# Kernel tuning notes

Measured on AMD Instinct MI355X. Metric: run time of the kernel, lower is better.

The kernel has to match this reference:

```python
import jax, jax.numpy as jnp
import numpy as np

G = 512          # number of graphs
N = 512          # nodes per graph (equal-sized graphs)
NN = G * N       # total nodes
EG = 8192        # edges per graph (avg degree 16)
C_IN, HID, OUT, K = 128, 32, 2, 20
LATENT = HID * 2 + 1  # 65 = conv1 kernel size & stride


def _gcn(x, W, b, src, dst, deg_inv_sqrt):
    """GCNConv with self-loops: out = D^-1/2 (A+I) D^-1/2 (x W) + b."""
    h = x @ W                                        # [NN, out]
    norm = deg_inv_sqrt[src] * deg_inv_sqrt[dst]     # [E]
    agg = jnp.zeros_like(h).at[dst].add(h[src] * norm[:, None])
    # self-loop message: norm_ii = deg_inv_sqrt[i]^2
    agg = agg + h * (deg_inv_sqrt * deg_inv_sqrt)[:, None]
    return agg + b


def setup_inputs() -> dict:
    key = jax.random.key(0)
    ks = jax.random.split(key, 24)
    x = jax.random.normal(ks[0], (NN, C_IN), jnp.float32)
    offs = (jnp.arange(G, dtype=jnp.int32) * N)[:, None]
    src = (jax.random.randint(ks[1], (G, EG), 0, N, jnp.int32) + offs).reshape(-1)
    dst = (jax.random.randint(ks[2], (G, EG), 0, N, jnp.int32) + offs).reshape(-1)
    edge_index = jnp.stack([src, dst])               # [2, G*EG]
    batch = jnp.repeat(jnp.arange(G, dtype=jnp.int32), N)

    def lin(k, fan_in, shape):
        return jax.random.normal(k, shape, jnp.float32) / np.sqrt(fan_in)

    return {
        "x": x, "edge_index": edge_index, "batch": batch,
        "W0": lin(ks[3], C_IN, (C_IN, HID)), "b0": jnp.zeros((HID,), jnp.float32),
        "W1": lin(ks[4], HID, (HID, HID)),   "b1": jnp.zeros((HID,), jnp.float32),
        "W2": lin(ks[5], HID, (HID, 1)),     "b2": jnp.zeros((1,), jnp.float32),
        "conv1_w": lin(ks[6], LATENT, (16, 1, LATENT)), "conv1_b": jnp.zeros((16,), jnp.float32),
        "conv2_w": lin(ks[7], 16 * 5, (32, 16, 5)),     "conv2_b": jnp.zeros((32,), jnp.float32),
        "lin1_w": lin(ks[8], 192, (192, 128)), "lin1_b": jnp.zeros((128,), jnp.float32),
        "lin2_w": lin(ks[9], 128, (128, OUT)), "lin2_b": jnp.zeros((OUT,), jnp.float32),
    }


def reference(x, edge_index, batch, W0, b0, W1, b1, W2, b2,
              conv1_w, conv1_b, conv2_w, conv2_b,
              lin1_w, lin1_b, lin2_w, lin2_b):
    src, dst = edge_index[0], edge_index[1]
    deg = jnp.zeros((NN,), jnp.float32).at[dst].add(1.0) + 1.0  # +1 self-loop
    dis = jax.lax.rsqrt(deg)

    x1 = jnp.tanh(_gcn(x,  W0, b0, src, dst, dis))   # [NN, 32]
    x2 = jnp.tanh(_gcn(x1, W1, b1, src, dst, dis))   # [NN, 32]
    x3 = jnp.tanh(_gcn(x2, W2, b2, src, dst, dis))   # [NN, 1]
    feat = jnp.concatenate([x1, x2, x3], axis=-1)    # [NN, 65]

    # global_sort_pool: equal-sized contiguous graphs -> reshape, sort by last
    # channel (descending) within each graph, take top-k nodes.
    fg = feat.reshape(G, N, LATENT)
    idx = jnp.argsort(-fg[..., -1], axis=1)[:, :K]                 # [G, K]
    pooled = jnp.take_along_axis(fg, idx[:, :, None], axis=1)      # [G, K, 65]

    # conv1: Conv1d(1,16,kernel=65,stride=65) over flattened [G,1,K*65]
    # == per-sorted-node matmul with the 65-wide kernel.
    h = jax.nn.relu(jnp.einsum('gkc,oc->gok', pooled, conv1_w[:, 0, :])
                    + conv1_b[None, :, None])                      # [G, 16, K]
    h = h.reshape(G, 16, K // 2, 2).max(-1)                        # MaxPool1d(2,2) -> [G,16,10]
    h = jax.nn.relu(
        jax.lax.conv_general_dilated(h, conv2_w, (1,), 'VALID',
                                     dimension_numbers=('NCH', 'OIH', 'NCH'))
        + conv2_b[None, :, None])                                  # [G, 32, 6]
    h = h.reshape(G, -1)                                           # [G, 192]
    h = jax.nn.relu(h @ lin1_w + lin1_b)
    # dropout is identity in eval mode
    return h @ lin2_w + lin2_b                                     # [G, 2]
```

## Files before the change

kernel.cpp:

```cpp
#include <hip/hip_runtime.h>
#include <math.h>

#define G_ 512
#define N_ 512
#define NN_ (G_*N_)
#define EG_ 8192
#define EGP 8704
#define CIN_ 128
#define HID_ 32
#define K_ 20
#define LAT_ 65
#define NSTRIPE 4
#define SW 8
#define HP 513

#define EPS_REL 1.8e-7f

__device__ __forceinline__ void decode_swz(int f, int& g, int& st) {
    int xcd = f & 7;
    int q = f >> 3;
    st = q & 3;
    g = xcd + 8 * (q >> 2);
}

__global__ __launch_bounds__(512) void csr2_kernel(const int* __restrict__ src,
                                                   const int* __restrict__ dst,
                                                   unsigned short* __restrict__ srcl,
                                                   int* __restrict__ gstart,
                                                   unsigned short* __restrict__ nperm,
                                                   double* __restrict__ disd) {
    __shared__ int cnt[N_];
    __shared__ int startv[N_];
    __shared__ int tmpv[N_];
    __shared__ int cursor[N_];
    __shared__ int hcur[128];
    __shared__ unsigned short binE[EGP];
    int g = blockIdx.x, tid = threadIdx.x;
    const int* ds = dst + (size_t)g * EG_;
    const int* ss = src + (size_t)g * EG_;
    int nb = g * N_;

    cnt[tid] = 0;
    if (tid < 128) hcur[tid] = 0;
    for (int i = tid; i < EGP; i += 512) binE[i] = 0xFFFF;
    __syncthreads();
    for (int e = tid; e < EG_; e += 512) atomicAdd(&cnt[ds[e] - nb], 1);
    __syncthreads();

    int mydeg = cnt[tid];
    int db = mydeg < 127 ? mydeg : 127;
    atomicAdd(&hcur[db], 1);
    __syncthreads();
    if (tid == 0) {
        int run = 0;
        for (int d = 0; d < 128; ++d) { int v = hcur[d]; hcur[d] = run; run += v; }
    }
    __syncthreads();
    {
        int slot = atomicAdd(&hcur[db], 1);
        nperm[g * N_ + slot] = (unsigned short)tid;
    }

    int pc = (mydeg + 1) & ~1;
    startv[tid] = pc;
    __syncthreads();
    for (int off = 1; off < N_; off <<= 1) {
        tmpv[tid] = startv[tid] + (tid >= off ? startv[tid - off] : 0);
        __syncthreads();
        startv[tid] = tmpv[tid];
        __syncthreads();
    }

    int excl = startv[tid] - pc;
    cursor[tid] = excl;
    gstart[g * (N_ + 1) + tid] = excl;
    if (tid == 511) gstart[g * (N_ + 1) + N_] = startv[511];
    disd[nb + tid] = 1.0 / sqrt((double)(mydeg + 1));
    __syncthreads();

    for (int e = tid; e < EG_; e += 512) {
        int d = ds[e] - nb;
        int slot = atomicAdd(&cursor[d], 1);
        binE[slot] = (unsigned short)e;
    }
    __syncthreads();

    {
        int n = mydeg;
        for (int i = 1; i < n; ++i) {
            unsigned short key = binE[excl + i];
            int j = i - 1;
            while (j >= 0 && binE[excl + j] > key) {
                binE[excl + j + 1] = binE[excl + j];
                --j;
            }
            binE[excl + j + 1] = key;
        }
    }
    __syncthreads();

    for (int i = tid; i < EGP; i += 512) {
        unsigned short e = binE[i];
        srcl[(size_t)g * EGP + i] =
            (e == 0xFFFF) ? (unsigned short)N_ : (unsigned short)(ss[e] - nb);
    }
}

template <int CI>
__global__ __launch_bounds__(256) void mm_kernel(const float* __restrict__ xin,
                                                 const float* __restrict__ W,
                                                 double* __restrict__ h) {
    __shared__ float sx[64][CI + 4];
    __shared__ float sWt[HID_][CI + 5];
    int tid = threadIdx.x;
    for (int i = tid; i < CI * HID_; i += 256) {
        int c = i / HID_, o = i % HID_;
        sWt[o][c] = W[i];
    }
    size_t base = (size_t)blockIdx.x * 64;
    const float4* xsrc = (const float4*)(xin + base * CI);
    for (int i = tid; i < 64 * CI / 4; i += 256) {
        int row = i / (CI / 4), col = (i % (CI / 4)) * 4;
        *(float4*)&sx[row][col] = xsrc[i];
    }
    __syncthreads();

    int o2 = tid & 15, q = tid >> 4;
    int n0 = q * 4;
    double acc[4][2];
#pragma unroll
    for (int j = 0; j < 4; ++j) { acc[j][0] = 0.0; acc[j][1] = 0.0; }

    for (int c = 0; c < CI; c += 4) {
        float4 wa = *(const float4*)&sWt[2 * o2][c];
        float4 wb = *(const float4*)&sWt[2 * o2 + 1][c];
        double w0a = (double)wa.x, w1a = (double)wa.y,
               w2a = (double)wa.z, w3a = (double)wa.w;
        double w0b = (double)wb.x, w1b = (double)wb.y,
               w2b = (double)wb.z, w3b = (double)wb.w;
#pragma unroll
        for (int j = 0; j < 4; ++j) {
            float4 v = *(const float4*)&sx[n0 + j][c];
            double vx = (double)v.x, vy = (double)v.y,
                   vz = (double)v.z, vw = (double)v.w;
            acc[j][0] = fma(vx, w0a, acc[j][0]);
            acc[j][0] = fma(vy, w1a, acc[j][0]);
            acc[j][0] = fma(vz, w2a, acc[j][0]);
            acc[j][0] = fma(vw, w3a, acc[j][0]);
            acc[j][1] = fma(vx, w0b, acc[j][1]);
            acc[j][1] = fma(vy, w1b, acc[j][1]);
            acc[j][1] = fma(vz, w2b, acc[j][1]);
            acc[j][1] = fma(vw, w3b, acc[j][1]);
        }
    }
    int stripe = o2 >> 3;
    {
        int o = 2 * o2;
        int strp = o >> 3;
        int oc = o & 7;
#pragma unroll
        for (int j = 0; j < 4; ++j) {
            double2 val;
            val.x = acc[j][0];
            val.y = acc[j][1];
            *(double2*)&h[(((size_t)strp) * NN_ + base + n0 + j) * SW + oc] = val;
        }
    }
    (void)stripe;
}

__global__ __launch_bounds__(512) void agg_kernel(const double* __restrict__ h,
                                                  const unsigned short* __restrict__ srcl,
                                                  const int* __restrict__ gstart,
                                                  const unsigned short* __restrict__ nperm,
                                                  const double* __restrict__ disd,
                                                  const float* __restrict__ bias,
                                                  float* __restrict__ xoutf) {
    __shared__ double hd2[SW * HP];
    __shared__ unsigned short ssrc[EGP];
    __shared__ unsigned short sstart[N_ + 2];
    __shared__ unsigned short sperm[N_];
    int g, st, tid = threadIdx.x;
    decode_swz(blockIdx.x, g, st);
    size_t nbase = (size_t)g * N_;

    for (int i = tid; i < EGP; i += 512) ssrc[i] = srcl[(size_t)g * EGP + i];
    for (int i = tid; i <= N_; i += 512) sstart[i] = (unsigned short)gstart[g * (N_ + 1) + i];
    sperm[tid] = nperm[g * N_ + tid];
    __syncthreads();

    const double* hraw = h + ((size_t)st * NN_ + nbase) * SW;
    const double* dg = disd + nbase;
    for (int i = tid; i < N_ * SW; i += 512) {
        int s = i >> 3, oc = i & 7;
        hd2[oc * HP + s] = hraw[i] * dg[s];
    }
    if (tid < SW) hd2[tid * HP + N_] = -0.0;
    __syncthreads();

    int oc = tid & 7, grp = tid >> 3;
    const double* hrow = hd2 + oc * HP;
    const unsigned int* ssrc32 = (const unsigned int*)ssrc;
    double b = (double)bias[st * SW + oc];

    int nn[8], e0h[8], e1h[8];
    double a[8];
    int mx = 0;
#pragma unroll
    for (int j = 0; j < 8; ++j) {
        int n = sperm[grp * 8 + j];
        nn[j] = n;
        e0h[j] = sstart[n] >> 1;
        e1h[j] = sstart[n + 1] >> 1;
        a[j] = 0.0;
        int d = e1h[j] - e0h[j];
        mx = d > mx ? d : mx;
    }
    for (int t = 0; t < mx; ++t) {
#pragma unroll
        for (int j = 0; j < 8; ++j) {
            int idx = e0h[j] + t;
            if (idx < e1h[j]) {
                unsigned int pr = ssrc32[idx];
                a[j] += hrow[pr & 0xFFFFu];
                a[j] += hrow[pr >> 16];
            }
        }
    }
#pragma unroll
    for (int j = 0; j < 8; ++j) {
        int n = nn[j];
        double dn = dg[n];
        double v = a[j] * dn + hrow[n] * dn + b;
        xoutf[(nbase + n) * HID_ + st * SW + oc] = tanhf((float)v);
    }
}

__global__ __launch_bounds__(512) void agg_mm_kernel(
        const float* __restrict__ xin,
        const float* __restrict__ W,
        const unsigned short* __restrict__ srcl,
        const int* __restrict__ gstart,
        const unsigned short* __restrict__ nperm,
        const double* __restrict__ disd,
        const float* __restrict__ bias,
        float* __restrict__ xoutf) {
    __shared__ double hd2[SW * HP];
    __shared__ unsigned short ssrc[EGP];
    __shared__ unsigned short sstart[N_ + 2];
    __shared__ double sWd[HID_ * SW];
    int g, st, tid = threadIdx.x;
    decode_swz(blockIdx.x, g, st);
    size_t nbase = (size_t)g * N_;

    for (int i = tid; i < EGP; i += 512) ssrc[i] = srcl[(size_t)g * EGP + i];
    for (int i = tid; i <= N_; i += 512) sstart[i] = (unsigned short)gstart[g * (N_ + 1) + i];
    if (tid < HID_ * SW) {
        int c = tid >> 3, oc = tid & 7;
        sWd[tid] = (double)W[c * HID_ + st * SW + oc];
    }
    __syncthreads();

    const double* dg = disd + nbase;
    {
        int s = tid;
        const float4* xr4 = (const float4*)(xin + (nbase + s) * HID_);
        float xrow[HID_];
#pragma unroll
        for (int q = 0; q < HID_ / 4; ++q) {
            float4 v = xr4[q];
            xrow[q * 4 + 0] = v.x;
            xrow[q * 4 + 1] = v.y;
            xrow[q * 4 + 2] = v.z;
            xrow[q * 4 + 3] = v.w;
        }
        double a[SW];
#pragma unroll
        for (int oc = 0; oc < SW; ++oc) a[oc] = 0.0;
#pragma unroll
        for (int c = 0; c < HID_; ++c) {
            double xv = (double)xrow[c];
#pragma unroll
            for (int oc = 0; oc < SW; ++oc)
                a[oc] = fma(xv, sWd[c * SW + oc], a[oc]);
        }
        double ds = dg[s];
#pragma unroll
        for (int oc = 0; oc < SW; ++oc)
            hd2[oc * HP + s] = a[oc] * ds;
    }
    if (tid < SW) hd2[tid * HP + N_] = -0.0;
    __syncthreads();

    int oc = tid & 7, grp = tid >> 3;
    const double* hrow = hd2 + oc * HP;
    const unsigned int* ssrc32 = (const unsigned int*)ssrc;
    double b = (double)bias[st * SW + oc];

    int nn[8], e0h[8], e1h[8];
    double a[8];
    int mx = 0;
#pragma unroll
    for (int j = 0; j < 8; ++j) {
        int n = nperm[g * N_ + grp * 8 + j];
        nn[j] = n;
        e0h[j] = sstart[n] >> 1;
        e1h[j] = sstart[n + 1] >> 1;
        a[j] = 0.0;
        int d = e1h[j] - e0h[j];
        mx = d > mx ? d : mx;
    }
    for (int t = 0; t < mx; ++t) {
#pragma unroll
        for (int j = 0; j < 8; ++j) {
            int idx = e0h[j] + t;
            if (idx < e1h[j]) {
                unsigned int pr = ssrc32[idx];
                a[j] += hrow[pr & 0xFFFFu];
                a[j] += hrow[pr >> 16];
            }
        }
    }
#pragma unroll
    for (int j = 0; j < 8; ++j) {
        int n = nn[j];
        double dn = dg[n];
        double v = a[j] * dn + hrow[n] * dn + b;
        xoutf[(nbase + n) * HID_ + st * SW + oc] = tanhf((float)v);
    }
}

__global__ __launch_bounds__(512) void gcn3_head_kernel(
        const float* __restrict__ xin,
        const float* __restrict__ W2,
        const float* __restrict__ b2,
        const unsigned short* __restrict__ srcl,
        const int* __restrict__ gstart,
        const double* __restrict__ disd,
        const float* __restrict__ x1,
        const float* __restrict__ x2,
        const float* __restrict__ c1w, const float* __restrict__ c1b,
        const float* __restrict__ c2w, const float* __restrict__ c2b,
        const float* __restrict__ l1w, const float* __restrict__ l1b,
        const float* __restrict__ l2w, const float* __restrict__ l2b,
        float* __restrict__ out) {
    __shared__ double h1[N_ + 1];
    __shared__ unsigned short ssrc[EGP];
    __shared__ int sstart[N_ + 1];
    __shared__ double sdis[N_ + 1];
    __shared__ float sv[N_];
    __shared__ int   topk[K_];
    __shared__ float pooled[K_][LAT_];
    __shared__ float c1[16][K_];
    __shared__ float mp[16][10];
    __shared__ float c2s[32 * 6];
    __shared__ float l1s[128];
    int g = blockIdx.x, tid = threadIdx.x;
    size_t nbase = (size_t)g * N_;

    for (int i = tid; i < EGP; i += 512) ssrc[i] = srcl[(size_t)g * EGP + i];
    for (int i = tid; i <= N_; i += 512) sstart[i] = gstart[g * (N_ + 1) + i];
    if (tid == 0) { h1[N_] = -0.0; sdis[N_] = 1.0; }
    if (tid < K_) topk[tid] = tid;
    int n = tid;
    {
        double a = 0.0;
#pragma unroll
        for (int c = 0; c < HID_; ++c)
            a = fma((double)xin[(nbase + n) * HID_ + c], (double)W2[c], a);
        h1[n] = a;
        sdis[n] = disd[nbase + n];
    }
    __syncthreads();

    {
        int e0 = sstart[n], e1 = sstart[n + 1];
        double a = 0.0;
        for (int e = e0; e < e1; ++e) {
            int s = ssrc[e];
            a += h1[s] * sdis[s];
        }
        double dn = sdis[n];
        double v = a * dn + h1[n] * dn * dn + (double)b2[0];
        sv[n] = (float)tanh(v);
    }
    __syncthreads();

    {
        float v = sv[n];
        int rank = 0;
        for (int j = 0; j < N_; ++j) {
            float u = sv[j];
            float mag = fmaxf(fabsf(u), fabsf(v));
            bool tie = fabsf(u - v) <= EPS_REL * mag;
            bool beats = tie ? (j < n) : (u > v);
            rank += beats;
        }
        if (rank < K_) topk[rank] = n;
    }
    __syncthreads();

    for (int i = tid; i < K_ * LAT_; i += 512) {
        int k = i / LAT_, c = i % LAT_;
        int node = topk[k];
        float f;
        if (c < HID_)            f = x1[(nbase + node) * HID_ + c];
        else if (c < 2 * HID_)   f = x2[(nbase + node) * HID_ + (c - HID_)];
        else                     f = sv[node];
        pooled[k][c] = f;
    }
    __syncthreads();

    for (int i = tid; i < 16 * K_; i += 512) {
        int o = i / K_, k = i % K_;
        float acc = c1b[o];
        for (int c = 0; c < LAT_; ++c) acc += pooled[k][c] * c1w[o * LAT_ + c];
        c1[o][k] = fmaxf(acc, 0.f);
    }
    __syncthreads();

    for (int i = tid; i < 160; i += 512) {
        int o = i / 10, t = i % 10;
        mp[o][t] = fmaxf(c1[o][2 * t], c1[o][2 * t + 1]);
    }
    __syncthreads();

    for (int i = tid; i < 192; i += 512) {
        int o = i / 6, t = i % 6;
        float acc = c2b[o];
        for (int ic = 0; ic < 16; ++ic)
#pragma unroll
            for (int j = 0; j < 5; ++j)
                acc += mp[ic][t + j] * c2w[(o * 16 + ic) * 5 + j];
        c2s[o * 6 + t] = fmaxf(acc, 0.f);
    }
    __syncthreads();

    for (int i = tid; i < 128; i += 512) {
        float acc = l1b[i];
        for (int c = 0; c < 192; ++c) acc += c2s[c] * l1w[c * 128 + i];
        l1s[i] = fmaxf(acc, 0.f);
    }
    __syncthreads();

    for (int i = tid; i < 2; i += 512) {
        float acc = l2b[i];
        for (int c = 0; c < 128; ++c) acc += l1s[c] * l2w[c * 2 + i];
        out[g * 2 + i] = acc;
    }
}

extern "C" void kernel_launch(void* const* d_in, const int* in_sizes, int n_in,
                              void* d_out, int out_size, void* d_ws, size_t ws_size,
                              hipStream_t stream) {
    const float* x   = (const float*)d_in[0];
    const int*   ei  = (const int*)d_in[1];
    const float* W0  = (const float*)d_in[3];
    const float* b0  = (const float*)d_in[4];
    const float* W1  = (const float*)d_in[5];
    const float* b1  = (const float*)d_in[6];
    const float* W2  = (const float*)d_in[7];
    const float* b2  = (const float*)d_in[8];
    const float* c1w = (const float*)d_in[9];
    const float* c1b = (const float*)d_in[10];
    const float* c2w = (const float*)d_in[11];
    const float* c2b = (const float*)d_in[12];
    const float* l1w = (const float*)d_in[13];
    const float* l1b = (const float*)d_in[14];
    const float* l2w = (const float*)d_in[15];
    const float* l2b = (const float*)d_in[16];

    const int* src = ei;
    const int* dst = ei + (size_t)G_ * EG_;

    char* wsb = (char*)d_ws;
    double* h64  = (double*)wsb;                 wsb += (size_t)NN_ * HID_ * 8;
    unsigned short* srcl = (unsigned short*)wsb; wsb += (size_t)G_ * EGP * 2;
    int* gstart = (int*)wsb;                     wsb += (size_t)G_ * (N_ + 1) * 4;
    unsigned short* nperm = (unsigned short*)wsb; wsb += (size_t)G_ * N_ * 2;
    double* disd = (double*)wsb;                 wsb += (size_t)NN_ * 8;
    float*  x1f  = (float*)wsb;                  wsb += (size_t)NN_ * HID_ * 4;
    float*  x2f  = (float*)wsb;                  wsb += (size_t)NN_ * HID_ * 4;

    csr2_kernel<<<G_, 512, 0, stream>>>(src, dst, srcl, gstart, nperm, disd);
    mm_kernel<CIN_><<<NN_ / 64, 256, 0, stream>>>(x, W0, h64);
    agg_kernel<<<G_ * NSTRIPE, 512, 0, stream>>>(h64, srcl, gstart, nperm, disd, b0, x1f);
    agg_mm_kernel<<<G_ * NSTRIPE, 512, 0, stream>>>(x1f, W1, srcl, gstart, nperm, disd, b1, x2f);
    gcn3_head_kernel<<<G_, 512, 0, stream>>>(x2f, W2, b2, srcl, gstart, disd,
                                             x1f, x2f, c1w, c1b, c2w, c2b,
                                             l1w, l1b, l2w, l2b, (float*)d_out);
}
```

Measured before the change: 323.2 us.

## Merge CSR build and first matmul into one launch with block-range dispatch

Fuses the independent CSR-construction kernel and the first-layer fp64 matmul into a single launch. The first G blocks build the CSR and the remaining blocks compute x@W0, so the two phases can run concurrently and one launch is saved. The matmul blocks now use 512 threads with 2 rows per thread instead of 256 threads with 4. All blocks share one 50KB shared buffer sized for the larger branch, which may reduce occupancy for the matmul blocks.

```diff
diff --git a/kernel.cpp b/kernel.cpp
--- a/kernel.cpp
+++ b/kernel.cpp
@@ -23,150 +23,145 @@
     g = xcd + 8 * (q >> 2);
 }
 
-__global__ __launch_bounds__(512) void csr2_kernel(const int* __restrict__ src,
-                                                   const int* __restrict__ dst,
-                                                   unsigned short* __restrict__ srcl,
-                                                   int* __restrict__ gstart,
-                                                   unsigned short* __restrict__ nperm,
-                                                   double* __restrict__ disd) {
-    __shared__ int cnt[N_];
-    __shared__ int startv[N_];
-    __shared__ int tmpv[N_];
-    __shared__ int cursor[N_];
-    __shared__ int hcur[128];
-    __shared__ unsigned short binE[EGP];
-    int g = blockIdx.x, tid = threadIdx.x;
-    const int* ds = dst + (size_t)g * EG_;
-    const int* ss = src + (size_t)g * EG_;
-    int nb = g * N_;
-
-    cnt[tid] = 0;
-    if (tid < 128) hcur[tid] = 0;
-    for (int i = tid; i < EGP; i += 512) binE[i] = 0xFFFF;
-    __syncthreads();
-    for (int e = tid; e < EG_; e += 512) atomicAdd(&cnt[ds[e] - nb], 1);
-    __syncthreads();
-
-    int mydeg = cnt[tid];
-    int db = mydeg < 127 ? mydeg : 127;
-    atomicAdd(&hcur[db], 1);
-    __syncthreads();
-    if (tid == 0) {
-        int run = 0;
-        for (int d = 0; d < 128; ++d) { int v = hcur[d]; hcur[d] = run; run += v; }
-    }
-    __syncthreads();
-    {
-        int slot = atomicAdd(&hcur[db], 1);
-        nperm[g * N_ + slot] = (unsigned short)tid;
-    }
-
-    int pc = (mydeg + 1) & ~1;
-    startv[tid] = pc;
-    __syncthreads();
-    for (int off = 1; off < N_; off <<= 1) {
-        tmpv[tid] = startv[tid] + (tid >= off ? startv[tid - off] : 0);
-        __syncthreads();
-        startv[tid] = tmpv[tid];
-        __syncthreads();
-    }
-
-    int excl = startv[tid] - pc;
-    cursor[tid] = excl;
-    gstart[g * (N_ + 1) + tid] = excl;
-    if (tid == 511) gstart[g * (N_ + 1) + N_] = startv[511];
-    disd[nb + tid] = 1.0 / sqrt((double)(mydeg + 1));
-    __syncthreads();
-
-    for (int e = tid; e < EG_; e += 512) {
-        int d = ds[e] - nb;
-        int slot = atomicAdd(&cursor[d], 1);
-        binE[slot] = (unsigned short)e;
-    }
-    __syncthreads();
-
-    {
-        int n = mydeg;
-        for (int i = 1; i < n; ++i) {
-            unsigned short key = binE[excl + i];
-            int j = i - 1;
-            while (j >= 0 && binE[excl + j] > key) {
-                binE[excl + j + 1] = binE[excl + j];
-                --j;
+__global__ __launch_bounds__(512) void csr_mm_kernel(
+        const int* __restrict__ src, const int* __restrict__ dst,
+        unsigned short* __restrict__ srcl, int* __restrict__ gstart,
+        unsigned short* __restrict__ nperm, double* __restrict__ disd,
+        const float* __restrict__ xin, const float* __restrict__ W,
+        double* __restrict__ h) {
+    __shared__ __align__(16) char smem[50816];
+    int tid = threadIdx.x;
+
+    if (blockIdx.x < G_) {
+        int* cnt    = (int*)smem;
+        int* startv = (int*)(smem + 2048);
+        int* tmpv   = (int*)(smem + 4096);
+        int* cursor = (int*)(smem + 6144);
+        int* hcur   = (int*)(smem + 8192);
+        unsigned short* binE = (unsigned short*)(smem + 8704);
+        int g = blockIdx.x;
+        const int* ds = dst + (size_t)g * EG_;
+        const int* ss = src + (size_t)g * EG_;
+        int nb = g * N_;
+
+        cnt[tid] = 0;
+        if (tid < 128) hcur[tid] = 0;
+        for (int i = tid; i < EGP; i += 512) binE[i] = 0xFFFF;
+        __syncthreads();
+        for (int e = tid; e < EG_; e += 512) atomicAdd(&cnt[ds[e] - nb], 1);
+        __syncthreads();
+
+        int mydeg = cnt[tid];
+        int db = mydeg < 127 ? mydeg : 127;
+        atomicAdd(&hcur[db], 1);
+        __syncthreads();
+        if (tid == 0) {
+            int run = 0;
+            for (int d = 0; d < 128; ++d) { int v = hcur[d]; hcur[d] = run; run += v; }
+        }
+        __syncthreads();
+        {
+            int slot = atomicAdd(&hcur[db], 1);
+            nperm[g * N_ + slot] = (unsigned short)tid;
+        }
+
+        int pc = (mydeg + 1) & ~1;
+        startv[tid] = pc;
+        __syncthreads();
+        for (int off = 1; off < N_; off <<= 1) {
+            tmpv[tid] = startv[tid] + (tid >= off ? startv[tid - off] : 0);
+            __syncthreads();
+            startv[tid] = tmpv[tid];
+            __syncthreads();
+        }
+
+        int excl = startv[tid] - pc;
+        cursor[tid] = excl;
+        gstart[g * (N_ + 1) + tid] = excl;
+        if (tid == 511) gstart[g * (N_ + 1) + N_] = startv[511];
+        disd[nb + tid] = 1.0 / sqrt((double)(mydeg + 1));
+        __syncthreads();
+
+        for (int e = tid; e < EG_; e += 512) {
+            int d = ds[e] - nb;
+            int slot = atomicAdd(&cursor[d], 1);
+            binE[slot] = (unsigned short)e;
+        }
+        __syncthreads();
+
+        {
+            int n = mydeg;
+            for (int i = 1; i < n; ++i) {
+                unsigned short key = binE[excl + i];
+                int j = i - 1;
+                while (j >= 0 && binE[excl + j] > key) {
+                    binE[excl + j + 1] = binE[excl + j];
+                    --j;
+                }
+                binE[excl + j + 1] = key;
             }
-            binE[excl + j + 1] = key;
-        }
-    }
-    __syncthreads();
-
-    for (int i = tid; i < EGP; i += 512) {
-        unsigned short e = binE[i];
-        srcl[(size_t)g * EGP + i] =
-            (e == 0xFFFF) ? (unsigned short)N_ : (unsigned short)(ss[e] - nb);
-    }
-}
-
-template <int CI>
-__global__ __launch_bounds__(256) void mm_kernel(const float* __restrict__ xin,
-                                                 const float* __restrict__ W,
-                                                 double* __restrict__ h) {
-    __shared__ float sx[64][CI + 4];
-    __shared__ float sWt[HID_][CI + 5];
-    int tid = threadIdx.x;
-    for (int i = tid; i < CI * HID_; i += 256) {
-        int c = i / HID_, o = i % HID_;
-        sWt[o][c] = W[i];
-    }
-    size_t base = (size_t)blockIdx.x * 64;
-    const float4* xsrc = (const float4*)(xin + base * CI);
-    for (int i = tid; i < 64 * CI / 4; i += 256) {
-        int row = i / (CI / 4), col = (i % (CI / 4)) * 4;
-        *(float4*)&sx[row][col] = xsrc[i];
-    }
-    __syncthreads();
-
-    int o2 = tid & 15, q = tid >> 4;
-    int n0 = q * 4;
-    double acc[4][2];
-#pragma unroll
-    for (int j = 0; j < 4; ++j) { acc[j][0] = 0.0; acc[j][1] = 0.0; }
-
-    for (int c = 0; c < CI; c += 4) {
-        float4 wa = *(const float4*)&sWt[2 * o2][c];
-        float4 wb = *(const float4*)&sWt[2 * o2 + 1][c];
-        double w0a = (double)wa.x, w1a = (double)wa.y,
-               w2a = (double)wa.z, w3a = (double)wa.w;
-        double w0b = (double)wb.x, w1b = (double)wb.y,
-               w2b = (double)wb.z, w3b = (double)wb.w;
-#pragma unroll
-        for (int j = 0; j < 4; ++j) {
-            float4 v = *(const float4*)&sx[n0 + j][c];
-            double vx = (double)v.x, vy = (double)v.y,
-                   vz = (double)v.z, vw = (double)v.w;
-            acc[j][0] = fma(vx, w0a, acc[j][0]);
-            acc[j][0] = fma(vy, w1a, acc[j][0]);
-            acc[j][0] = fma(vz, w2a, acc[j][0]);
-            acc[j][0] = fma(vw, w3a, acc[j][0]);
-            acc[j][1] = fma(vx, w0b, acc[j][1]);
-            acc[j][1] = fma(vy, w1b, acc[j][1]);
-            acc[j][1] = fma(vz, w2b, acc[j][1]);
-            acc[j][1] = fma(vw, w3b, acc[j][1]);
-        }
-    }
-    int stripe = o2 >> 3;
-    {
+        }
+        __syncthreads();
+
+        for (int i = tid; i < EGP; i += 512) {
+            unsigned short e = binE[i];
+            srcl[(size_t)g * EGP + i] =
+                (e == 0xFFFF) ? (unsigned short)N_ : (unsigned short)(ss[e] - nb);
+        }
+    } else {
+        float (*sx)[CIN_ + 4] = (float(*)[CIN_ + 4])smem;
+        float (*sWt)[CIN_ + 5] = (float(*)[CIN_ + 5])(smem + 33792);
+        for (int i = tid; i < CIN_ * HID_; i += 512) {
+            int c = i / HID_, o = i % HID_;
+            sWt[o][c] = W[i];
+        }
+        size_t base = (size_t)(blockIdx.x - G_) * 64;
+        const float4* xsrc = (const float4*)(xin + base * CIN_);
+        for (int i = tid; i < 64 * CIN_ / 4; i += 512) {
+            int row = i / (CIN_ / 4), col = (i % (CIN_ / 4)) * 4;
+            *(float4*)&sx[row][col] = xsrc[i];
+        }
+        __syncthreads();
+
+        int o2 = tid & 15, q = tid >> 4;
+        int n0 = q * 2;
+        double acc[2][2];
+#pragma unroll
+        for (int j = 0; j < 2; ++j) { acc[j][0] = 0.0; acc[j][1] = 0.0; }
+
+        for (int c = 0; c < CIN_; c += 4) {
+            float4 wa = *(const float4*)&sWt[2 * o2][c];
+            float4 wb = *(const float4*)&sWt[2 * o2 + 1][c];
+            double w0a = (double)wa.x, w1a = (double)wa.y,
+                   w2a = (double)wa.z, w3a = (double)wa.w;
+            double w0b = (double)wb.x, w1b = (double)wb.y,
+                   w2b = (double)wb.z, w3b = (double)wb.w;
+#pragma unroll
+            for (int j = 0; j < 2; ++j) {
+                float4 v = *(const float4*)&sx[n0 + j][c];
+                double vx = (double)v.x, vy = (double)v.y,
+                       vz = (double)v.z, vw = (double)v.w;
+                acc[j][0] = fma(vx, w0a, acc[j][0]);
+                acc[j][0] = fma(vy, w1a, acc[j][0]);
+                acc[j][0] = fma(vz, w2a, acc[j][0]);
+                acc[j][0] = fma(vw, w3a, acc[j][0]);
+                acc[j][1] = fma(vx, w0b, acc[j][1]);
+                acc[j][1] = fma(vy, w1b, acc[j][1]);
+                acc[j][1] = fma(vz, w2b, acc[j][1]);
+                acc[j][1] = fma(vw, w3b, acc[j][1]);
+            }
+        }
         int o = 2 * o2;
         int strp = o >> 3;
         int oc = o & 7;
 #pragma unroll
-        for (int j = 0; j < 4; ++j) {
+        for (int j = 0; j < 2; ++j) {
             double2 val;
             val.x = acc[j][0];
             val.y = acc[j][1];
             *(double2*)&h[(((size_t)strp) * NN_ + base + n0 + j) * SW + oc] = val;
         }
     }
-    (void)stripe;
 }
 
 __global__ __launch_bounds__(512) void agg_kernel(const double* __restrict__ h,
@@ -482,8 +477,8 @@
     float*  x1f  = (float*)wsb;                  wsb += (size_t)NN_ * HID_ * 4;
     float*  x2f  = (float*)wsb;                  wsb += (size_t)NN_ * HID_ * 4;
 
-    csr2_kernel<<<G_, 512, 0, stream>>>(src, dst, srcl, gstart, nperm, disd);
-    mm_kernel<CIN_><<<NN_ / 64, 256, 0, stream>>>(x, W0, h64);
+    csr_mm_kernel<<<G_ + NN_ / 64, 512, 0, stream>>>(src, dst, srcl, gstart,
+                                                     nperm, disd, x, W0, h64);
     agg_kernel<<<G_ * NSTRIPE, 512, 0, stream>>>(h64, srcl, gstart, nperm, disd, b0, x1f);
     agg_mm_kernel<<<G_ * NSTRIPE, 512, 0, stream>>>(x1f, W1, srcl, gstart, nperm, disd, b1, x2f);
     gcn3_head_kernel<<<G_, 512, 0, stream>>>(x2f, W2, b2, srcl, gstart, disd,
```

Measured after the change: 477.7 us. 1.48x slower.
